# Kernel optimization log

Hardware: AMD Instinct MI355X
Metric: run time of the kernel (lower is better)

## Reference

```python
import jax, jax.numpy as jnp
import numpy as np

LEVELS = 100
TIMESTAMPS = 32768
DIM = 2048
N = 32768
SIG_MIN, SIG_MAX = -3.0, 3.0


def _bipolar(key, shape):
    return jnp.where(jax.random.uniform(key, shape) < 0.5, -1.0, 1.0).astype(jnp.float32)


def setup_inputs() -> dict:
    key = jax.random.key(0)
    ks = jax.random.split(key, 11)
    # (t, x, y, z): sorted times in [0, TIMESTAMPS), gaussian signals
    times = jnp.sort(jax.random.uniform(ks[0], (N,), minval=0.0, maxval=float(TIMESTAMPS)))
    # ensure strictly increasing so jerk dt != 0
    times = times + jnp.arange(N, dtype=jnp.float32) * 1e-3
    xyz = jax.random.normal(ks[1], (N, 3), dtype=jnp.float32)
    inp = jnp.concatenate([times[:, None], xyz], axis=1)  # [N,4]
    return {
        "input": inp,
        "W_x": _bipolar(ks[2], (LEVELS, DIM)),
        "W_y": _bipolar(ks[3], (LEVELS, DIM)),
        "W_z": _bipolar(ks[4], (LEVELS, DIM)),
        "W_mag": _bipolar(ks[5], (LEVELS, DIM)),
        "W_xj": _bipolar(ks[6], (LEVELS, DIM)),
        "W_yj": _bipolar(ks[7], (LEVELS, DIM)),
        "W_zj": _bipolar(ks[8], (LEVELS, DIM)),
        "W_magj": _bipolar(ks[9], (LEVELS, DIM)),
        "W_t": _bipolar(ks[10], (TIMESTAMPS, DIM)),
    }


def _level_lookup(table, value, low, high):
    # torchhd Level: map value in [low, high] to index in [0, n-1], clamp, gather
    n = table.shape[0]
    idx = jnp.round((value - low) / (high - low) * (n - 1)).astype(jnp.int32)
    idx = jnp.clip(idx, 0, n - 1)
    return table[idx]  # [N, DIM]


def reference(input, W_x, W_y, W_z, W_mag, W_xj, W_yj, W_zj, W_magj, W_t):
    t = input[:, 0] - input[0, 0]
    x = jnp.clip(input[:, 1], SIG_MIN, SIG_MAX)
    y = jnp.clip(input[:, 2], SIG_MIN, SIG_MAX)
    z = jnp.clip(input[:, 3], SIG_MIN, SIG_MAX)
    x_lv = _level_lookup(W_x, x, SIG_MIN, SIG_MAX)
    y_lv = _level_lookup(W_y, y, SIG_MIN, SIG_MAX)
    z_lv = _level_lookup(W_z, z, SIG_MIN, SIG_MAX)
    mags = jnp.sqrt(jnp.sum(input[:, 1:] ** 2, axis=1))
    mag_lv = _level_lookup(W_mag, mags, SIG_MIN, SIG_MAX)
    # vectorized jerk: row 0 is zeros (matches the original's initial zeros row)
    dt = t[1:] - t[:-1]
    jerk = jnp.concatenate(
        [jnp.zeros((1, 3), input.dtype), (input[1:, 1:] - input[:-1, 1:]) / dt[:, None]],
        axis=0,
    )  # [N,3]
    xj = jnp.clip(jerk[:, 0], SIG_MIN, SIG_MAX)
    yj = jnp.clip(jerk[:, 1], SIG_MIN, SIG_MAX)
    zj = jnp.clip(jerk[:, 2], SIG_MIN, SIG_MAX)
    xj_lv = _level_lookup(W_xj, xj, SIG_MIN, SIG_MAX)
    yj_lv = _level_lookup(W_yj, yj, SIG_MIN, SIG_MAX)
    zj_lv = _level_lookup(W_zj, zj, SIG_MIN, SIG_MAX)
    jmag = jnp.sqrt(jnp.sum(jerk ** 2, axis=1))
    jmag_lv = _level_lookup(W_magj, jmag, SIG_MIN, SIG_MAX)
    t_lv = _level_lookup(W_t, t, 0.0, float(TIMESTAMPS))
    sample_hvs = ((x_lv + y_lv + z_lv) * mag_lv + (xj_lv + yj_lv + zj_lv) * jmag_lv) * t_lv
    return jnp.tanh(jnp.sum(sample_hvs, axis=0))  # [DIM] multiset + tanh
```

## Files before the change

### kernel.cpp

```cpp
#include <hip/hip_runtime.h>
#include <hip/hip_bf16.h>
#include <math.h>

#define DIM     2048
#define LEVELS  100
#define TSN     32768
#define NBLK    1024
#define NSPLIT  32
#define PACK_BLOCKS 200

__device__ __forceinline__ int lvl100(float v) {
    float f = ((v + 3.0f) / 6.0f) * 99.0f;
    int k = (int)rintf(f);
    return min(max(k, 0), LEVELS - 1);
}

__global__ __launch_bounds__(256) void prep_k(
    const float* __restrict__ w0, const float* __restrict__ w1,
    const float* __restrict__ w2, const float* __restrict__ w3,
    const float* __restrict__ w4, const float* __restrict__ w5,
    const float* __restrict__ w6, const float* __restrict__ w7,
    const float* __restrict__ inp,
    unsigned int* __restrict__ packed2,
    unsigned long long* __restrict__ sidx,
    unsigned int* __restrict__ tidx, int n)
{
    if (blockIdx.x < PACK_BLOCKS) {
        int tab = blockIdx.x / 25;
        int lg  = blockIdx.x - tab * 25;
        int l   = threadIdx.x & 63;
        int level = lg * 4 + (threadIdx.x >> 6);
        const float* w;
        switch (tab) {
            case 0: w = w0; break; case 1: w = w1; break;
            case 2: w = w2; break; case 3: w = w3; break;
            case 4: w = w4; break; case 5: w = w5; break;
            case 6: w = w6; break; default: w = w7; break;
        }
        const float* base = w + (size_t)level * DIM + 4 * l;
        unsigned int word = 0;
        #pragma unroll
        for (int k = 0; k < 8; ++k) {
            float4 a = *(const float4*)(base + 256 * k);
            word |= (a.x < 0.f ? 1u : 0u) << (4 * k);
            word |= (a.y < 0.f ? 1u : 0u) << (4 * k + 1);
            word |= (a.z < 0.f ? 1u : 0u) << (4 * k + 2);
            word |= (a.w < 0.f ? 1u : 0u) << (4 * k + 3);
        }
        packed2[(tab * LEVELS + level) * 64 + l] = word;
        return;
    }
    int i = (blockIdx.x - PACK_BLOCKS) * 256 + threadIdx.x;
    if (i >= n) return;
    float t0 = inp[0];
    float ti = inp[i * 4] - t0;
    float x = inp[i * 4 + 1], y = inp[i * 4 + 2], z = inp[i * 4 + 3];
    float xc = fminf(fmaxf(x, -3.f), 3.f);
    float yc = fminf(fmaxf(y, -3.f), 3.f);
    float zc = fminf(fmaxf(z, -3.f), 3.f);
    unsigned long long ix = (unsigned long long)lvl100(xc);
    unsigned long long iy = (unsigned long long)lvl100(yc);
    unsigned long long iz = (unsigned long long)lvl100(zc);
    float mag = sqrtf((x * x + y * y) + z * z);
    unsigned long long im = (unsigned long long)lvl100(mag);
    float jx = 0.f, jy = 0.f, jz = 0.f;
    if (i > 0) {
        float tp = inp[(i - 1) * 4] - t0;
        float dt = ti - tp;
        jx = (x - inp[(i - 1) * 4 + 1]) / dt;
        jy = (y - inp[(i - 1) * 4 + 2]) / dt;
        jz = (z - inp[(i - 1) * 4 + 3]) / dt;
    }
    unsigned long long ixj = (unsigned long long)lvl100(fminf(fmaxf(jx, -3.f), 3.f));
    unsigned long long iyj = (unsigned long long)lvl100(fminf(fmaxf(jy, -3.f), 3.f));
    unsigned long long izj = (unsigned long long)lvl100(fminf(fmaxf(jz, -3.f), 3.f));
    float jm = sqrtf((jx * jx + jy * jy) + jz * jz);
    unsigned long long imj = (unsigned long long)lvl100(jm);
    sidx[i] = ix | (iy << 8) | (iz << 16) | (im << 24) |
              (ixj << 32) | (iyj << 40) | (izj << 48) | (imj << 56);
    float ft = (ti / 32768.0f) * 32767.0f;
    int k = (int)rintf(ft);
    tidx[i] = (unsigned int)min(max(k, 0), TSN - 1);
}

__global__ __launch_bounds__(256) void main_k(
    const float* __restrict__ Wt,
    const unsigned int* __restrict__ packed2,
    const unsigned long long* __restrict__ sidx,
    const unsigned int* __restrict__ tidx,
    float* __restrict__ partials, int spw, int n)
{
    __shared__ float red[4][DIM];
    const int tid = threadIdx.x;
    const int l   = tid & 63;
    const int wv  = tid >> 6;
    int gw = blockIdx.x * 4 + wv;
    int s0 = gw * spw;
    int s1 = min(s0 + spw, n);

    float4 acc[8];
    #pragma unroll
    for (int k = 0; k < 8; ++k) acc[k] = make_float4(0.f, 0.f, 0.f, 0.f);

    #pragma unroll 2
    for (int s = s0; s < s1; ++s) {
        int su = __builtin_amdgcn_readfirstlane(s);
        unsigned long long sp = sidx[su];
        unsigned int ti = tidx[su];
        const float4* rowp = (const float4*)(Wt + (size_t)ti * DIM);

        unsigned int i_x  = (unsigned int)(sp)       & 0xffu;
        unsigned int i_y  = (unsigned int)(sp >> 8)  & 0xffu;
        unsigned int i_z  = (unsigned int)(sp >> 16) & 0xffu;
        unsigned int i_m  = (unsigned int)(sp >> 24) & 0xffu;
        unsigned int i_xj = (unsigned int)(sp >> 32) & 0xffu;
        unsigned int i_yj = (unsigned int)(sp >> 40) & 0xffu;
        unsigned int i_zj = (unsigned int)(sp >> 48) & 0xffu;
        unsigned int i_mj = (unsigned int)(sp >> 56) & 0xffu;

        unsigned int Bx  = packed2[(0 * LEVELS + i_x ) * 64 + l];
        unsigned int By  = packed2[(1 * LEVELS + i_y ) * 64 + l];
        unsigned int Bz  = packed2[(2 * LEVELS + i_z ) * 64 + l];
        unsigned int Bm  = packed2[(3 * LEVELS + i_m ) * 64 + l];
        unsigned int Bxj = packed2[(4 * LEVELS + i_xj) * 64 + l];
        unsigned int Byj = packed2[(5 * LEVELS + i_yj) * 64 + l];
        unsigned int Bzj = packed2[(6 * LEVELS + i_zj) * 64 + l];
        unsigned int Bmj = packed2[(7 * LEVELS + i_mj) * 64 + l];

        unsigned int e1 = Bx ^ Bm,  e2 = By ^ Bm,  e3 = Bz ^ Bm;
        unsigned int e4 = Bxj ^ Bmj, e5 = Byj ^ Bmj, e6 = Bzj ^ Bmj;
        unsigned int ta  = e1 ^ e2;
        unsigned int sA  = ta ^ e3;
        unsigned int cA  = (e1 & e2) | (e3 & ta);
        unsigned int tb2 = e4 ^ e5;
        unsigned int sB  = tb2 ^ e6;
        unsigned int cB  = (e4 & e5) | (e6 & tb2);
        unsigned int ones  = sA ^ sB;
        unsigned int cc    = sA & sB;
        unsigned int tc    = cA ^ cB;
        unsigned int twos  = tc ^ cc;
        unsigned int fours = (cA & cB) | (cc & tc);

        #pragma unroll
        for (int k = 0; k < 8; ++k) {
            float4 wt4 = rowp[64 * k + l];
            #pragma unroll
            for (int j = 0; j < 4; ++j) {
                int p = 4 * k + j;
                int v = ((ones >> p) & 1) + 2 * ((twos >> p) & 1)
                      + 4 * ((fours >> p) & 1);
                float sgn = (float)(6 - 2 * v);
                float* a = (float*)&acc[k];
                float* wf = (float*)&wt4;
                a[j] = fmaf(sgn, wf[j], a[j]);
            }
        }
    }

    float4* redw = (float4*)red[wv];
    #pragma unroll
    for (int k = 0; k < 8; ++k) redw[64 * k + l] = acc[k];
    __syncthreads();

    float4 o0 = make_float4(0.f, 0.f, 0.f, 0.f);
    float4 o1 = make_float4(0.f, 0.f, 0.f, 0.f);
    #pragma unroll
    for (int r = 0; r < 4; ++r) {
        float4 a = ((float4*)red[r])[2 * tid];
        float4 b = ((float4*)red[r])[2 * tid + 1];
        o0.x += a.x; o0.y += a.y; o0.z += a.z; o0.w += a.w;
        o1.x += b.x; o1.y += b.y; o1.z += b.z; o1.w += b.w;
    }
    float4* pout = (float4*)(partials + (size_t)blockIdx.x * DIM + tid * 8);
    pout[0] = o0;
    pout[1] = o1;
}

__global__ __launch_bounds__(256) void reduce1_k(
    const float* __restrict__ partials, float* __restrict__ partial2,
    int rows_per, int nblk)
{
    int d = blockIdx.x * 256 + threadIdx.x;
    int r0 = blockIdx.y * rows_per;
    int r1 = min(r0 + rows_per, nblk);
    float s = 0.f;
    for (int b = r0; b < r1; ++b) s += partials[(size_t)b * DIM + d];
    partial2[(size_t)blockIdx.y * DIM + d] = s;
}

__global__ __launch_bounds__(256) void reduce2_k(
    const float* __restrict__ partial2, float* __restrict__ out)
{
    int d = blockIdx.x * 256 + threadIdx.x;
    float s = 0.f;
    #pragma unroll
    for (int b = 0; b < NSPLIT; ++b) s += partial2[(size_t)b * DIM + d];
    out[d] = tanhf(s);
}

extern "C" void kernel_launch(void* const* d_in, const int* in_sizes, int n_in,
                              void* d_out, int out_size, void* d_ws, size_t ws_size,
                              hipStream_t stream)
{
    const float* inp = (const float*)d_in[0];
    const float* wx  = (const float*)d_in[1];
    const float* wy  = (const float*)d_in[2];
    const float* wz  = (const float*)d_in[3];
    const float* wm  = (const float*)d_in[4];
    const float* wxj = (const float*)d_in[5];
    const float* wyj = (const float*)d_in[6];
    const float* wzj = (const float*)d_in[7];
    const float* wmj = (const float*)d_in[8];
    const float* wt  = (const float*)d_in[9];
    int n = in_sizes[0] / 4;

    char* ws = (char*)d_ws;
    unsigned int* packed2 = (unsigned int*)ws;
    size_t off = 256 * 1024;
    unsigned long long* sidx = (unsigned long long*)(ws + off);
    off += (size_t)n * 8;
    unsigned int* tidx = (unsigned int*)(ws + off);
    off += (size_t)n * 4;
    off = (off + 255) & ~(size_t)255;

    float* partial2 = (float*)(ws + off);
    off += (size_t)NSPLIT * DIM * 4;

    int nblk = NBLK;
    while (nblk > 32 && off + (size_t)nblk * DIM * 4 > ws_size) nblk >>= 1;
    float* partials = (float*)(ws + off);

    int idx_blocks = (n + 255) / 256;
    hipLaunchKernelGGL(prep_k, dim3(PACK_BLOCKS + idx_blocks), dim3(256), 0, stream,
                       wx, wy, wz, wm, wxj, wyj, wzj, wmj,
                       inp, packed2, sidx, tidx, n);
    int spw = (n + nblk * 4 - 1) / (nblk * 4);
    hipLaunchKernelGGL(main_k, dim3(nblk), dim3(256), 0, stream,
                       wt, packed2, sidx, tidx, partials, spw, n);
    int rows_per = (nblk + NSPLIT - 1) / NSPLIT;
    hipLaunchKernelGGL(reduce1_k, dim3(DIM / 256, NSPLIT), dim3(256), 0, stream,
                       partials, partial2, rows_per, nblk);
    hipLaunchKernelGGL(reduce2_k, dim3(DIM / 256), dim3(256), 0, stream,
                       partial2, (float*)d_out);
}
```

Measured before the change: 55.33 us.

## Fuse first-stage reduction into main kernel via atomic adds to split rows

Each main-kernel block now atomically adds its 2048-wide partial sum into one of 32 accumulator rows, chosen by block index modulo 32. This replaces the separate per-block partials buffer and the reduce1 kernel launch. The accumulator rows are zeroed by extra blocks in the prep kernel. This removes one kernel launch and an 8 MB write-then-read of partials, at the cost of float atomic contention (32 blocks per row) and a nondeterministic summation order.

```diff
diff --git a/kernel.cpp b/kernel.cpp
--- a/kernel.cpp
+++ b/kernel.cpp
@@ -8,6 +8,7 @@
 #define NBLK    1024
 #define NSPLIT  32
 #define PACK_BLOCKS 200
+#define ZERO_BLOCKS 32
 
 __device__ __forceinline__ int lvl100(float v) {
     float f = ((v + 3.0f) / 6.0f) * 99.0f;
@@ -23,7 +24,8 @@
     const float* __restrict__ inp,
     unsigned int* __restrict__ packed2,
     unsigned long long* __restrict__ sidx,
-    unsigned int* __restrict__ tidx, int n)
+    unsigned int* __restrict__ tidx,
+    float* __restrict__ partial2, int n)
 {
     if (blockIdx.x < PACK_BLOCKS) {
         int tab = blockIdx.x / 25;
@@ -50,7 +52,15 @@
         packed2[(tab * LEVELS + level) * 64 + l] = word;
         return;
     }
-    int i = (blockIdx.x - PACK_BLOCKS) * 256 + threadIdx.x;
+    if (blockIdx.x < PACK_BLOCKS + ZERO_BLOCKS) {
+        int row = blockIdx.x - PACK_BLOCKS;
+        float4 z = make_float4(0.f, 0.f, 0.f, 0.f);
+        float4* p = (float4*)(partial2 + (size_t)row * DIM);
+        p[threadIdx.x] = z;
+        p[threadIdx.x + 256] = z;
+        return;
+    }
+    int i = (blockIdx.x - PACK_BLOCKS - ZERO_BLOCKS) * 256 + threadIdx.x;
     if (i >= n) return;
     float t0 = inp[0];
     float ti = inp[i * 4] - t0;
@@ -88,7 +98,7 @@
     const unsigned int* __restrict__ packed2,
     const unsigned long long* __restrict__ sidx,
     const unsigned int* __restrict__ tidx,
-    float* __restrict__ partials, int spw, int n)
+    float* __restrict__ partial2, int spw, int n)
 {
     __shared__ float red[4][DIM];
     const int tid = threadIdx.x;
@@ -171,21 +181,11 @@
         o0.x += a.x; o0.y += a.y; o0.z += a.z; o0.w += a.w;
         o1.x += b.x; o1.y += b.y; o1.z += b.z; o1.w += b.w;
     }
-    float4* pout = (float4*)(partials + (size_t)blockIdx.x * DIM + tid * 8);
-    pout[0] = o0;
-    pout[1] = o1;
-}
-
-__global__ __launch_bounds__(256) void reduce1_k(
-    const float* __restrict__ partials, float* __restrict__ partial2,
-    int rows_per, int nblk)
-{
-    int d = blockIdx.x * 256 + threadIdx.x;
-    int r0 = blockIdx.y * rows_per;
-    int r1 = min(r0 + rows_per, nblk);
-    float s = 0.f;
-    for (int b = r0; b < r1; ++b) s += partials[(size_t)b * DIM + d];
-    partial2[(size_t)blockIdx.y * DIM + d] = s;
+    float* prow = partial2 + (size_t)(blockIdx.x & (NSPLIT - 1)) * DIM + tid * 8;
+    atomicAdd(prow + 0, o0.x); atomicAdd(prow + 1, o0.y);
+    atomicAdd(prow + 2, o0.z); atomicAdd(prow + 3, o0.w);
+    atomicAdd(prow + 4, o1.x); atomicAdd(prow + 5, o1.y);
+    atomicAdd(prow + 6, o1.z); atomicAdd(prow + 7, o1.w);
 }
 
 __global__ __launch_bounds__(256) void reduce2_k(
@@ -222,24 +222,17 @@
     unsigned int* tidx = (unsigned int*)(ws + off);
     off += (size_t)n * 4;
     off = (off + 255) & ~(size_t)255;
-
     float* partial2 = (float*)(ws + off);
     off += (size_t)NSPLIT * DIM * 4;
 
-    int nblk = NBLK;
-    while (nblk > 32 && off + (size_t)nblk * DIM * 4 > ws_size) nblk >>= 1;
-    float* partials = (float*)(ws + off);
-
     int idx_blocks = (n + 255) / 256;
-    hipLaunchKernelGGL(prep_k, dim3(PACK_BLOCKS + idx_blocks), dim3(256), 0, stream,
+    hipLaunchKernelGGL(prep_k,
+                       dim3(PACK_BLOCKS + ZERO_BLOCKS + idx_blocks), dim3(256), 0, stream,
                        wx, wy, wz, wm, wxj, wyj, wzj, wmj,
-                       inp, packed2, sidx, tidx, n);
-    int spw = (n + nblk * 4 - 1) / (nblk * 4);
-    hipLaunchKernelGGL(main_k, dim3(nblk), dim3(256), 0, stream,
-                       wt, packed2, sidx, tidx, partials, spw, n);
-    int rows_per = (nblk + NSPLIT - 1) / NSPLIT;
-    hipLaunchKernelGGL(reduce1_k, dim3(DIM / 256, NSPLIT), dim3(256), 0, stream,
-                       partials, partial2, rows_per, nblk);
+                       inp, packed2, sidx, tidx, partial2, n);
+    int spw = (n + NBLK * 4 - 1) / (NBLK * 4);
+    hipLaunchKernelGGL(main_k, dim3(NBLK), dim3(256), 0, stream,
+                       wt, packed2, sidx, tidx, partial2, spw, n);
     hipLaunchKernelGGL(reduce2_k, dim3(DIM / 256), dim3(256), 0, stream,
                        partial2, (float*)d_out);
 }
```

Result: slower. 87.22 us (+57.6%).
